# Performance work log

Measured on AMD Instinct MI355X. Metric: run time of the kernel, lower is better.

Reference implementation:

```python
import math
import jax, jax.numpy as jnp
import numpy as np

D_MODEL = 2048
NUM_HEADS = 16
HEAD_DIM = 128
MIN_PERIOD = 0.01
MAX_PERIOD = 10.0
LN_EPS = 1e-5


def temporal_pos_enc(num_frames, frame_interval, d_model, dtype):
    # frame times in seconds, sin-cos encoding with log-spaced periods.
    times = jnp.arange(num_frames, dtype=jnp.float32) * frame_interval  # [N]
    fraction = jnp.linspace(0.0, 1.0, d_model // 2, dtype=jnp.float32)  # [D/2]
    period = MIN_PERIOD * (MAX_PERIOD / MIN_PERIOD) ** fraction
    scaling = (2.0 * math.pi) / period                                  # [D/2]
    sin_in = times[:, None] * scaling[None, :]                          # [N, D/2]
    enc = jnp.concatenate([jnp.sin(sin_in), jnp.cos(sin_in)], axis=1)   # [N, D]
    return enc.astype(dtype)


def setup_inputs() -> dict:
    key = jax.random.key(0)
    ks = jax.random.split(key, 7)
    B, N, S, L_other, D = 4, 4, 768, 48, D_MODEL
    HD = NUM_HEADS * HEAD_DIM
    seq_len = N * S + L_other
    scale = 1.0 / math.sqrt(D)
    return {
        "hidden_states": jax.random.normal(ks[0], (B, seq_len, D), jnp.float32),
        "Wq": jax.random.normal(ks[1], (HD, D), jnp.float32) * scale,
        "Wk": jax.random.normal(ks[2], (HD, D), jnp.float32) * scale,
        "Wv": jax.random.normal(ks[3], (HD, D), jnp.float32) * scale,
        "Wo": jax.random.normal(ks[4], (D, HD), jnp.float32) * scale,
        "ln_gamma": jnp.ones((D,), jnp.float32),
        "ln_beta": jnp.zeros((D,), jnp.float32),
        "num_image_tokens_per_frame": 768,
        "num_frames": 4,
        "frame_interval": 0.1,
    }


def reference(hidden_states, Wq, Wk, Wv, Wo, ln_gamma, ln_beta,
              num_image_tokens_per_frame, num_frames, frame_interval):
    B, seq_len, D = hidden_states.shape
    S = num_image_tokens_per_frame
    N = num_frames
    T = S * N
    H, hd = NUM_HEADS, HEAD_DIM
    scaling = hd ** (-0.5)

    img = hidden_states[:, :T, :]           # [B, T, D]
    other = hidden_states[:, T:, :]         # [B, L_other, D]
    residual = img

    # fp32 LayerNorm
    x32 = img.astype(jnp.float32)
    mu = jnp.mean(x32, axis=-1, keepdims=True)
    var = jnp.mean(jnp.square(x32 - mu), axis=-1, keepdims=True)
    x = ((x32 - mu) * jax.lax.rsqrt(var + LN_EPS) * ln_gamma + ln_beta).astype(hidden_states.dtype)

    # [B, N, S, D] + temporal pos enc broadcast over batch & space
    x = x.reshape(B, N, S, D)
    x = x + temporal_pos_enc(N, frame_interval, D, x.dtype)[None, :, None, :]
    x = jnp.transpose(x, (0, 2, 1, 3))      # [B, S, N, D]

    # QKV projections (Linear: y = x @ W.T)
    q = jnp.einsum('bsnd,ed->bsne', x, Wq).reshape(B, S, N, H, hd)
    k = jnp.einsum('bsnd,ed->bsne', x, Wk).reshape(B, S, N, H, hd)
    v = jnp.einsum('bsnd,ed->bsne', x, Wv).reshape(B, S, N, H, hd)

    # attention over temporal axis (n, m are frame indices)
    scores = jnp.einsum('bsnhd,bsmhd->bshnm', q, k) * scaling
    attn = jax.nn.softmax(scores.astype(jnp.float32), axis=-1).astype(q.dtype)
    out = jnp.einsum('bshnm,bsmhd->bsnhd', attn, v)   # [B, S, N, H, hd]
    out = out.reshape(B, S, N, H * hd)
    out = jnp.einsum('bsne,de->bsnd', out, Wo)        # [B, S, N, D]

    out = jnp.transpose(out, (0, 2, 1, 3)).reshape(B, N * S, D)
    img_out = residual + out
    return jnp.concatenate([img_out, other], axis=1)
```

## Files before the change

### kernel.cpp

```cpp
#include <hip/hip_runtime.h>
#include <hip/hip_bf16.h>
#include <math.h>

#define BATCH 4
#define NFRM  4
#define STOK  768
#define TIMG  3072
#define SEQ   3120
#define DM    2048
#define NH    16
#define HDIM  128
#define MTOK  12288

typedef __attribute__((ext_vector_type(8))) short short8;
typedef __attribute__((ext_vector_type(4))) float f32x4;

__device__ __forceinline__ unsigned short f2bf(float f) {
  unsigned u = __float_as_uint(f);
  u += 0x7FFF + ((u >> 16) & 1);
  return (unsigned short)(u >> 16);
}
__device__ __forceinline__ float bf2f(unsigned short s) {
  return __uint_as_float(((unsigned)s) << 16);
}

__device__ __forceinline__ void gload_lds16(const void* g, void* l) {
  __builtin_amdgcn_global_load_lds(
      (const __attribute__((address_space(1))) void*)g,
      (__attribute__((address_space(3))) void*)l,
      16, 0, 0);
}

__global__ void k_enc(const float* __restrict__ fi, float* __restrict__ enc) {
  int i = blockIdx.x * 256 + threadIdx.x;
  if (i >= NFRM * DM) return;
  int n = i >> 11;
  int d = i & (DM - 1);
  int dd = d & 1023;
  float fraction = dd * (1.0f / 1023.0f);
  float period = 0.01f * powf(1000.0f, fraction);
  float sc = 6.283185307179586f / period;
  float x = (n * fi[0]) * sc;
  enc[i] = (d < 1024) ? sinf(x) : cosf(x);
}

__global__ void k_wconv(const float4* __restrict__ Wq, const float4* __restrict__ Wk,
                        const float4* __restrict__ Wv, const float4* __restrict__ Wo,
                        unsigned short* __restrict__ wqkv, unsigned short* __restrict__ wo) {
  int id = blockIdx.x * 256 + threadIdx.x;
  int mat = id >> 20;
  int j = id & 1048575;
  const float4* src = (mat == 0) ? Wq : (mat == 1) ? Wk : (mat == 2) ? Wv : Wo;
  float4 v = src[j];
  ushort4 o4;
  o4.x = f2bf(v.x); o4.y = f2bf(v.y); o4.z = f2bf(v.z); o4.w = f2bf(v.w);
  unsigned short* dst = (mat < 3) ? (wqkv + (size_t)mat * 4194304) : wo;
  *(ushort4*)&dst[(size_t)j * 4] = o4;
}

__global__ __launch_bounds__(256)
void k_ln(const float* __restrict__ hid, const float* __restrict__ gamma,
          const float* __restrict__ beta, const float* __restrict__ enc,
          unsigned short* __restrict__ X) {
  int token = blockIdx.x;
  int b = token / TIMG;
  int t = token - b * TIMG;
  int n = t / STOK;
  const float* row = hid + (size_t)(b * SEQ + t) * DM;
  int tid = threadIdx.x;

  float xv[8];
  *(float4*)&xv[0] = *(const float4*)&row[tid * 8];
  *(float4*)&xv[4] = *(const float4*)&row[tid * 8 + 4];

  float s = 0.f, ss = 0.f;
#pragma unroll
  for (int j = 0; j < 8; ++j) { s += xv[j]; ss += xv[j] * xv[j]; }
#pragma unroll
  for (int mask = 32; mask >= 1; mask >>= 1) {
    s += __shfl_xor(s, mask);
    ss += __shfl_xor(ss, mask);
  }
  __shared__ float ps[4], pss[4];
  int lane = tid & 63, wid = tid >> 6;
  if (lane == 0) { ps[wid] = s; pss[wid] = ss; }
  __syncthreads();
  s = ps[0] + ps[1] + ps[2] + ps[3];
  ss = pss[0] + pss[1] + pss[2] + pss[3];

  float mean = s * (1.0f / DM);
  float var = ss * (1.0f / DM) - mean * mean;
  float inv = rsqrtf(var + 1e-5f);

  float gv[8], bv[8], ev[8];
  *(float4*)&gv[0] = *(const float4*)&gamma[tid * 8];
  *(float4*)&gv[4] = *(const float4*)&gamma[tid * 8 + 4];
  *(float4*)&bv[0] = *(const float4*)&beta[tid * 8];
  *(float4*)&bv[4] = *(const float4*)&beta[tid * 8 + 4];
  *(float4*)&ev[0] = *(const float4*)&enc[n * DM + tid * 8];
  *(float4*)&ev[4] = *(const float4*)&enc[n * DM + tid * 8 + 4];

  short8 outv;
#pragma unroll
  for (int j = 0; j < 8; ++j) {
    float y = (xv[j] - mean) * inv * gv[j] + bv[j] + ev[j];
    outv[j] = (short)f2bf(y);
  }
  *(short8*)&X[(size_t)token * DM + tid * 8] = outv;
}

template <int EPI>
__global__ __launch_bounds__(256)
void gemm_bt(const unsigned short* __restrict__ A, const unsigned short* __restrict__ B,
             unsigned short* __restrict__ Cb, float* __restrict__ Cf,
             const float* __restrict__ resid, int M, int N, int K) {
  __shared__ unsigned short ldsA[128 * 32];
  __shared__ unsigned short ldsB[128 * 32];
  const int tid = threadIdx.x;
  const int lane = tid & 63;
  const int wid = tid >> 6;
  const int tm = blockIdx.y * 128;
  const int tn = blockIdx.x * 128;
  const int l16 = lane & 15;
  const int kq = lane >> 4;
  const int wr = (wid >> 1) * 64;
  const int wc = (wid & 1) * 64;

  f32x4 zero = {0.f, 0.f, 0.f, 0.f};
  f32x4 acc[4][4];
#pragma unroll
  for (int i = 0; i < 4; ++i)
#pragma unroll
    for (int j = 0; j < 4; ++j) acc[i][j] = zero;

  const int c0 = wid * 64 + lane;
  const int r0 = c0 >> 2, s0 = c0 & 3;
  const int c1 = 256 + c0;
  const int r1 = c1 >> 2, s1 = c1 & 3;

  const unsigned short* ga0 = A + (size_t)(tm + r0) * K + s0 * 8;
  const unsigned short* ga1 = A + (size_t)(tm + r1) * K + s1 * 8;
  const unsigned short* gb0 = B + (size_t)(tn + r0) * K + s0 * 8;
  const unsigned short* gb1 = B + (size_t)(tn + r1) * K + s1 * 8;
  char* la0 = (char*)ldsA + (wid * 64) * 16;
  char* la1 = (char*)ldsA + (256 + wid * 64) * 16;
  char* lb0 = (char*)ldsB + (wid * 64) * 16;
  char* lb1 = (char*)ldsB + (256 + wid * 64) * 16;

  for (int k0 = 0; k0 < K; k0 += 32) {
    __syncthreads();
    gload_lds16(ga0 + k0, la0);
    gload_lds16(ga1 + k0, la1);
    gload_lds16(gb0 + k0, lb0);
    gload_lds16(gb1 + k0, lb1);
    __syncthreads();

    short8 a[4], b[4];
#pragma unroll
    for (int mi = 0; mi < 4; ++mi)
      a[mi] = *(const short8*)&ldsA[(wr + mi * 16 + l16) * 32 + kq * 8];
#pragma unroll
    for (int ni = 0; ni < 4; ++ni)
      b[ni] = *(const short8*)&ldsB[(wc + ni * 16 + l16) * 32 + kq * 8];
#pragma unroll
    for (int mi = 0; mi < 4; ++mi)
#pragma unroll
      for (int ni = 0; ni < 4; ++ni)
        acc[mi][ni] = __builtin_amdgcn_mfma_f32_16x16x32_bf16(a[mi], b[ni], acc[mi][ni], 0, 0, 0);
  }

#pragma unroll
  for (int mi = 0; mi < 4; ++mi) {
#pragma unroll
    for (int ni = 0; ni < 4; ++ni) {
      int row0 = tm + wr + mi * 16 + kq * 4;
      int colg = tn + wc + ni * 16 + l16;
#pragma unroll
      for (int r = 0; r < 4; ++r) {
        int row = row0 + r;
        float val = acc[mi][ni][r];
        if (EPI == 0) {
          Cb[(size_t)row * N + colg] = f2bf(val);
        } else {
          int bb = row / TIMG;
          int t = row - bb * TIMG;
          size_t o = (size_t)(bb * SEQ + t) * DM + colg;
          Cf[o] = resid[o] + val;
        }
      }
    }
  }
}

__global__ __launch_bounds__(256)
void k_attn(const unsigned short* __restrict__ QKV, unsigned short* __restrict__ AOUT) {
  int bs = blockIdx.x;
  int b = bs / STOK;
  int s = bs - b * STOK;
  int tid = threadIdx.x;
  int h = tid >> 4;
  int part = tid & 15;
  int col = h * HDIM + part * 8;

  float q[4][8], k[4][8], v[4][8];
#pragma unroll
  for (int n = 0; n < 4; ++n) {
    size_t base = (size_t)(b * TIMG + n * STOK + s) * 6144;
    short8 qa = *(const short8*)&QKV[base + col];
    short8 ka = *(const short8*)&QKV[base + 2048 + col];
    short8 va = *(const short8*)&QKV[base + 4096 + col];
#pragma unroll
    for (int j = 0; j < 8; ++j) {
      q[n][j] = bf2f((unsigned short)qa[j]);
      k[n][j] = bf2f((unsigned short)ka[j]);
      v[n][j] = bf2f((unsigned short)va[j]);
    }
  }

  float sc[4][4];
#pragma unroll
  for (int n = 0; n < 4; ++n)
#pragma unroll
    for (int m = 0; m < 4; ++m) {
      float a = 0.f;
#pragma unroll
      for (int j = 0; j < 8; ++j) a += q[n][j] * k[m][j];
#pragma unroll
      for (int mask = 8; mask >= 1; mask >>= 1) a += __shfl_xor(a, mask);
      sc[n][m] = a * 0.08838834764831845f;
    }

  float p[4][4];
#pragma unroll
  for (int n = 0; n < 4; ++n) {
    float mx = fmaxf(fmaxf(sc[n][0], sc[n][1]), fmaxf(sc[n][2], sc[n][3]));
    float sum = 0.f;
#pragma unroll
    for (int m = 0; m < 4; ++m) { p[n][m] = expf(sc[n][m] - mx); sum += p[n][m]; }
    float inv = 1.f / sum;
#pragma unroll
    for (int m = 0; m < 4; ++m) p[n][m] *= inv;
  }

#pragma unroll
  for (int n = 0; n < 4; ++n) {
    float o[8];
#pragma unroll
    for (int j = 0; j < 8; ++j) o[j] = 0.f;
#pragma unroll
    for (int m = 0; m < 4; ++m)
#pragma unroll
      for (int j = 0; j < 8; ++j) o[j] += p[n][m] * v[m][j];
    short8 ov;
#pragma unroll
    for (int j = 0; j < 8; ++j) ov[j] = (short)f2bf(o[j]);
    size_t obase = (size_t)(b * TIMG + n * STOK + s) * DM + col;
    *(short8*)&AOUT[obase] = ov;
  }
}

__global__ void k_other(const float4* __restrict__ hid, float4* __restrict__ out) {
  int i = blockIdx.x * 256 + threadIdx.x;
  int b = i / 24576;
  int r = i - b * 24576;
  size_t off = ((size_t)(b * SEQ + TIMG) * DM) / 4 + r;
  out[off] = hid[off];
}

extern "C" void kernel_launch(void* const* d_in, const int* in_sizes, int n_in,
                              void* d_out, int out_size, void* d_ws, size_t ws_size,
                              hipStream_t stream) {
  const float* hid   = (const float*)d_in[0];
  const float* Wq    = (const float*)d_in[1];
  const float* Wk    = (const float*)d_in[2];
  const float* Wv    = (const float*)d_in[3];
  const float* Wo    = (const float*)d_in[4];
  const float* gamma = (const float*)d_in[5];
  const float* beta  = (const float*)d_in[6];
  const float* fint  = (const float*)d_in[9];
  float* out = (float*)d_out;

  char* ws = (char*)d_ws;
  float*          enc  = (float*)(ws + 0);
  unsigned short* wqkv = (unsigned short*)(ws + 32768);
  unsigned short* wo   = (unsigned short*)(ws + 25198592);
  unsigned short* X    = (unsigned short*)(ws + 33587200);
  unsigned short* QKV  = (unsigned short*)(ws + 83918848);
  unsigned short* aout = X;

  k_enc<<<32, 256, 0, stream>>>(fint, enc);
  k_wconv<<<16384, 256, 0, stream>>>((const float4*)Wq, (const float4*)Wk,
                                     (const float4*)Wv, (const float4*)Wo, wqkv, wo);
  k_ln<<<MTOK, 256, 0, stream>>>(hid, gamma, beta, enc, X);
  gemm_bt<0><<<dim3(48, 96), 256, 0, stream>>>(X, wqkv, QKV, nullptr, nullptr,
                                               MTOK, 6144, DM);
  k_attn<<<BATCH * STOK, 256, 0, stream>>>(QKV, aout);
  gemm_bt<1><<<dim3(16, 96), 256, 0, stream>>>(aout, wo, nullptr, out, hid,
                                               MTOK, DM, DM);
  k_other<<<384, 256, 0, stream>>>((const float4*)hid, (float4*)out);
}
```

Baseline: 837.0 us.

## Replace 128x128 GEMM with double-buffered 256x256 swizzled-LDS MFMA kernel

Both projection GEMMs move to a new kernel with 256x256 output tiles, 512 threads and a 64-wide K step. It double-buffers A/B tiles in 128KB of LDS, using direct global-to-LDS loads, an XOR-swizzled layout and vmcnt-based waits. It also remaps the 1D grid so neighbouring tiles are grouped, and raises wave priority around the MFMA bursts. The aims are more operand reuse per LDS load, fewer bank conflicts and overlap of loads with compute. The cost is heavy LDS and register use, so each CU holds only one workgroup.

Result: faster. 705.7 us (-15.7%).

```diff
diff --git a/kernel.cpp b/kernel.cpp
--- a/kernel.cpp
+++ b/kernel.cpp
@@ -29,6 +29,12 @@
       (const __attribute__((address_space(1))) void*)g,
       (__attribute__((address_space(3))) void*)l,
       16, 0, 0);
+}
+
+__device__ __forceinline__ void barrier_fenced() {
+  asm volatile("" ::: "memory");
+  __builtin_amdgcn_s_barrier();
+  asm volatile("" ::: "memory");
 }
 
 __global__ void k_enc(const float* __restrict__ fi, float* __restrict__ enc) {
@@ -110,81 +116,119 @@
 }
 
 template <int EPI>
-__global__ __launch_bounds__(256)
-void gemm_bt(const unsigned short* __restrict__ A, const unsigned short* __restrict__ B,
+__global__ __launch_bounds__(512, 2)
+void gemm256(const unsigned short* __restrict__ A, const unsigned short* __restrict__ B,
              unsigned short* __restrict__ Cb, float* __restrict__ Cf,
-             const float* __restrict__ resid, int M, int N, int K) {
-  __shared__ unsigned short ldsA[128 * 32];
-  __shared__ unsigned short ldsB[128 * 32];
+             const float* __restrict__ resid, int M, int N, int K, int nbx) {
+  __shared__ char lds[131072];
+
+  const int nwg = gridDim.x;
+  const int q = nwg >> 3;
+  const int bid = blockIdx.x;
+  const int swz = (bid & 7) * q + (bid >> 3);
+  const int by = swz / nbx;
+  const int bx = swz - by * nbx;
+  const int tm = by * 256, tn = bx * 256;
+
   const int tid = threadIdx.x;
   const int lane = tid & 63;
   const int wid = tid >> 6;
-  const int tm = blockIdx.y * 128;
-  const int tn = blockIdx.x * 128;
+  const int wm = wid >> 2;
+  const int wn = wid & 3;
   const int l16 = lane & 15;
   const int kq = lane >> 4;
-  const int wr = (wid >> 1) * 64;
-  const int wc = (wid & 1) * 64;
-
-  f32x4 zero = {0.f, 0.f, 0.f, 0.f};
-  f32x4 acc[4][4];
-#pragma unroll
-  for (int i = 0; i < 4; ++i)
-#pragma unroll
-    for (int j = 0; j < 4; ++j) acc[i][j] = zero;
-
-  const int c0 = wid * 64 + lane;
-  const int r0 = c0 >> 2, s0 = c0 & 3;
-  const int c1 = 256 + c0;
-  const int r1 = c1 >> 2, s1 = c1 & 3;
-
-  const unsigned short* ga0 = A + (size_t)(tm + r0) * K + s0 * 8;
-  const unsigned short* ga1 = A + (size_t)(tm + r1) * K + s1 * 8;
-  const unsigned short* gb0 = B + (size_t)(tn + r0) * K + s0 * 8;
-  const unsigned short* gb1 = B + (size_t)(tn + r1) * K + s1 * 8;
-  char* la0 = (char*)ldsA + (wid * 64) * 16;
-  char* la1 = (char*)ldsA + (256 + wid * 64) * 16;
-  char* lb0 = (char*)ldsB + (wid * 64) * 16;
-  char* lb1 = (char*)ldsB + (256 + wid * 64) * 16;
-
-  for (int k0 = 0; k0 < K; k0 += 32) {
-    __syncthreads();
-    gload_lds16(ga0 + k0, la0);
-    gload_lds16(ga1 + k0, la1);
-    gload_lds16(gb0 + k0, lb0);
-    gload_lds16(gb1 + k0, lb1);
-    __syncthreads();
-
-    short8 a[4], b[4];
-#pragma unroll
-    for (int mi = 0; mi < 4; ++mi)
-      a[mi] = *(const short8*)&ldsA[(wr + mi * 16 + l16) * 32 + kq * 8];
+
+  const int srow = tid >> 3;
+  const int sslot = tid & 7;
+  const unsigned short* gA[4];
+  const unsigned short* gB[4];
+#pragma unroll
+  for (int i = 0; i < 4; ++i) {
+    int row = i * 64 + srow;
+    int lslot = sslot ^ (row & 7);
+    gA[i] = A + (size_t)(tm + row) * K + lslot * 8;
+    gB[i] = B + (size_t)(tn + row) * K + lslot * 8;
+  }
+
+  f32x4 acc[8][4];
+#pragma unroll
+  for (int i = 0; i < 8; ++i)
+#pragma unroll
+    for (int j = 0; j < 4; ++j) acc[i][j] = (f32x4){0.f, 0.f, 0.f, 0.f};
+
+  auto STAGE = [&](int k0, int buf) {
+    char* base = lds + buf * 65536 + wid * 1024;
+#pragma unroll
+    for (int i = 0; i < 4; ++i) gload_lds16(gA[i] + k0, base + i * 8192);
+#pragma unroll
+    for (int i = 0; i < 4; ++i) gload_lds16(gB[i] + k0, base + 32768 + i * 8192);
+  };
+
+  auto COMPUTE = [&](int buf) {
+    const char* pa = lds + buf * 65536;
+    const char* pb = pa + 32768;
+    short8 breg[4][2];
 #pragma unroll
     for (int ni = 0; ni < 4; ++ni)
-      b[ni] = *(const short8*)&ldsB[(wc + ni * 16 + l16) * 32 + kq * 8];
-#pragma unroll
-    for (int mi = 0; mi < 4; ++mi)
-#pragma unroll
-      for (int ni = 0; ni < 4; ++ni)
-        acc[mi][ni] = __builtin_amdgcn_mfma_f32_16x16x32_bf16(a[mi], b[ni], acc[mi][ni], 0, 0, 0);
-  }
-
-#pragma unroll
-  for (int mi = 0; mi < 4; ++mi) {
+#pragma unroll
+      for (int ks = 0; ks < 2; ++ks) {
+        int row = wn * 64 + ni * 16 + l16;
+        int slot = (ks * 4 + kq) ^ (row & 7);
+        breg[ni][ks] = *(const short8*)(pb + row * 128 + slot * 16);
+      }
+#pragma unroll
+    for (int p = 0; p < 4; ++p) {
+      short8 areg[2][2];
+#pragma unroll
+      for (int mi = 0; mi < 2; ++mi)
+#pragma unroll
+        for (int ks = 0; ks < 2; ++ks) {
+          int row = wm * 128 + (p * 2 + mi) * 16 + l16;
+          int slot = (ks * 4 + kq) ^ (row & 7);
+          areg[mi][ks] = *(const short8*)(pa + row * 128 + slot * 16);
+        }
+      __builtin_amdgcn_s_setprio(1);
+#pragma unroll
+      for (int mi = 0; mi < 2; ++mi)
+#pragma unroll
+        for (int ni = 0; ni < 4; ++ni)
+#pragma unroll
+          for (int ks = 0; ks < 2; ++ks)
+            acc[p * 2 + mi][ni] = __builtin_amdgcn_mfma_f32_16x16x32_bf16(
+                areg[mi][ks], breg[ni][ks], acc[p * 2 + mi][ni], 0, 0, 0);
+      __builtin_amdgcn_s_setprio(0);
+    }
+  };
+
+  const int NT = K >> 6;
+  STAGE(0, 0);
+  for (int t = 0; t < NT - 1; ++t) {
+    STAGE((t + 1) << 6, (t + 1) & 1);
+    asm volatile("s_waitcnt vmcnt(8)" ::: "memory");
+    barrier_fenced();
+    COMPUTE(t & 1);
+    barrier_fenced();
+  }
+  asm volatile("s_waitcnt vmcnt(0)" ::: "memory");
+  barrier_fenced();
+  COMPUTE((NT - 1) & 1);
+
+#pragma unroll
+  for (int mi = 0; mi < 8; ++mi) {
 #pragma unroll
     for (int ni = 0; ni < 4; ++ni) {
-      int row0 = tm + wr + mi * 16 + kq * 4;
-      int colg = tn + wc + ni * 16 + l16;
+      int row0 = tm + wm * 128 + mi * 16 + kq * 4;
+      int col = tn + wn * 64 + ni * 16 + l16;
 #pragma unroll
       for (int r = 0; r < 4; ++r) {
         int row = row0 + r;
         float val = acc[mi][ni][r];
         if (EPI == 0) {
-          Cb[(size_t)row * N + colg] = f2bf(val);
+          Cb[(size_t)row * N + col] = f2bf(val);
         } else {
           int bb = row / TIMG;
-          int t = row - bb * TIMG;
-          size_t o = (size_t)(bb * SEQ + t) * DM + colg;
+          int t2 = row - bb * TIMG;
+          size_t o = (size_t)(bb * SEQ + t2) * DM + col;
           Cf[o] = resid[o] + val;
         }
       }
@@ -292,10 +336,10 @@
   k_wconv<<<16384, 256, 0, stream>>>((const float4*)Wq, (const float4*)Wk,
                                      (const float4*)Wv, (const float4*)Wo, wqkv, wo);
   k_ln<<<MTOK, 256, 0, stream>>>(hid, gamma, beta, enc, X);
-  gemm_bt<0><<<dim3(48, 96), 256, 0, stream>>>(X, wqkv, QKV, nullptr, nullptr,
-                                               MTOK, 6144, DM);
+  gemm256<0><<<1152, 512, 0, stream>>>(X, wqkv, QKV, nullptr, nullptr,
+                                       MTOK, 6144, DM, 24);
   k_attn<<<BATCH * STOK, 256, 0, stream>>>(QKV, aout);
-  gemm_bt<1><<<dim3(16, 96), 256, 0, stream>>>(aout, wo, nullptr, out, hid,
-                                               MTOK, DM, DM);
+  gemm256<1><<<384, 512, 0, stream>>>(aout, wo, nullptr, out, hid,
+                                      MTOK, DM, DM, 8);
   k_other<<<384, 256, 0, stream>>>((const float4*)hid, (float4*)out);
 }
```
